# Optimization experiments

Hardware: AMD Instinct MI355X
Metric: run time of the kernel (lower is better)

Reference implementation:

```python
import jax, jax.numpy as jnp
import numpy as np

T, B = 64, 256
VOCAB, D, H = 32000, 512, 1024


def setup_inputs() -> dict:
    key = jax.random.key(0)
    k1, k2, k3, k4 = jax.random.split(key, 4)
    x = jax.random.randint(k1, (T, B), 0, VOCAB)  # token 0 = padding
    embed = jax.random.normal(k2, (VOCAB, D), dtype=jnp.float32)
    w_i = jax.random.normal(k3, (D, 3 * H), dtype=jnp.float32) / np.sqrt(D)
    w_h = jax.random.normal(k4, (H, 3 * H), dtype=jnp.float32) / np.sqrt(H)
    b = jnp.zeros((3 * H,), dtype=jnp.float32)
    return {"x": x, "embed": embed, "w_i": w_i, "w_h": w_h, "b": b}


def reference(x, embed, w_i, w_h, b):
    # Embed and mask out padding token 0.  words: [T, B, D]
    words = embed[x] * (x > 0).astype(embed.dtype)[..., None]
    h_dim = w_h.shape[0]
    w_h_zr, w_h_a = w_h[:, : 2 * h_dim], w_h[:, 2 * h_dim :]
    b_zr, b_a = b[: 2 * h_dim], b[2 * h_dim :]

    def step(h, w_t):
        gx = w_t @ w_i  # [B, 3H]
        zr_x, a_x = gx[..., : 2 * h_dim], gx[..., 2 * h_dim :]
        zr = jax.nn.sigmoid(zr_x + h @ w_h_zr + b_zr)
        z, r = zr[..., :h_dim], zr[..., h_dim:]
        a = jnp.tanh(a_x + (r * h) @ w_h_a + b_a)
        h_new = (1.0 - z) * h + z * a
        return h_new, h_new

    h0 = jnp.zeros((x.shape[1], h_dim), dtype=embed.dtype)
    _, seq = jax.lax.scan(step, h0, words)  # seq: [T, B, H]
    return seq.sum(0)  # compress == 'sum' -> [B, H]
```

## Files before the change

### kernel.cpp

```cpp
#include <hip/hip_runtime.h>
#include <hip/hip_bf16.h>
#include <stdint.h>


#define TT 64
#define BB 256
#define DD 512
#define HH 1024
#define N3H 3072

using frag  = __attribute__((ext_vector_type(8))) short;
using f32x4 = __attribute__((ext_vector_type(4))) float;

__device__ __forceinline__ uint16_t f2b(float f) {
    uint32_t u = __builtin_bit_cast(uint32_t, f);
    uint32_t r = u + 0x7FFFu + ((u >> 16) & 1u);
    return (uint16_t)(r >> 16);
}
__device__ __forceinline__ float b2f(uint16_t b) {
    uint32_t u = ((uint32_t)b) << 16;
    return __builtin_bit_cast(float, u);
}

__device__ __forceinline__ void load8_issue(const uint16_t* p, frag* f) {
    asm volatile(
        "global_load_dwordx4 %0, %8, off sc0 sc1\n\t"
        "global_load_dwordx4 %1, %8, off offset:64 sc0 sc1\n\t"
        "global_load_dwordx4 %2, %8, off offset:128 sc0 sc1\n\t"
        "global_load_dwordx4 %3, %8, off offset:192 sc0 sc1\n\t"
        "global_load_dwordx4 %4, %8, off offset:256 sc0 sc1\n\t"
        "global_load_dwordx4 %5, %8, off offset:320 sc0 sc1\n\t"
        "global_load_dwordx4 %6, %8, off offset:384 sc0 sc1\n\t"
        "global_load_dwordx4 %7, %8, off offset:448 sc0 sc1"
        : "=&v"(f[0]), "=&v"(f[1]), "=&v"(f[2]), "=&v"(f[3]),
          "=&v"(f[4]), "=&v"(f[5]), "=&v"(f[6]), "=&v"(f[7])
        : "v"(p)
        : "memory");
}

#define WAIT8(N, F)                                                       \
    asm volatile("s_waitcnt vmcnt(" #N ")"                                \
                 : "+v"((F)[0]), "+v"((F)[1]), "+v"((F)[2]),              \
                   "+v"((F)[3]), "+v"((F)[4]), "+v"((F)[5]),              \
                   "+v"((F)[6]), "+v"((F)[7]))

#define ZCON(KB, HF)                                                              \
    _Pragma("unroll")                                                             \
    for (int j = 0; j < 8; ++j) {                                                 \
        int kk = (KB) * 8 + j;                                                    \
        frag b0 = *(const frag*)(Wh + (l16)      * LDW + kk * 32 + quad * 8);     \
        frag b1 = *(const frag*)(Wh + (16 + l16) * LDW + kk * 32 + quad * 8);     \
        acc0 = __builtin_amdgcn_mfma_f32_16x16x32_bf16((HF)[j], b0, acc0, 0, 0, 0); \
        acc1 = __builtin_amdgcn_mfma_f32_16x16x32_bf16((HF)[j], b1, acc1, 0, 0, 0); \
    }

#define ACON(KB, RF)                                                              \
    _Pragma("unroll")                                                             \
    for (int j = 0; j < 8; ++j) {                                                 \
        int kk = (KB) * 8 + j;                                                    \
        frag b2 = *(const frag*)(Wh + (32 + l16) * LDW + kk * 32 + quad * 8);     \
        acc2 = __builtin_amdgcn_mfma_f32_16x16x32_bf16((RF)[j], b2, acc2, 0, 0, 0); \
    }


__global__ __launch_bounds__(256) void k_gather(const int* __restrict__ x,
                                                const float* __restrict__ embed,
                                                uint16_t* __restrict__ words) {
    int tid = blockIdx.x * 256 + threadIdx.x;
    int row = tid >> 6;
    int c8  = (tid & 63) << 3;
    int tok = x[row];
    float s = (tok > 0) ? 1.f : 0.f;
    const float4* src = (const float4*)(embed + (int64_t)tok * DD + c8);
    float4 v0 = src[0], v1 = src[1];
    float vals[8] = {v0.x, v0.y, v0.z, v0.w, v1.x, v1.y, v1.z, v1.w};
    union { uint16_t u[8]; uint4 q; } pk;
#pragma unroll
    for (int i = 0; i < 8; ++i) pk.u[i] = f2b(vals[i] * s);
    *(uint4*)(words + ((int64_t)row << 9) + c8) = pk.q;
}

__global__ void k_transpose(const float* __restrict__ src, uint16_t* __restrict__ dst,
                            int K, int N) {
    __shared__ float tile[32][33];
    int n0 = blockIdx.x * 32, k0 = blockIdx.y * 32;
    int tx = threadIdx.x, ty = threadIdx.y;
#pragma unroll
    for (int i = 0; i < 32; i += 8)
        tile[ty + i][tx] = src[(int64_t)(k0 + ty + i) * N + n0 + tx];
    __syncthreads();
#pragma unroll
    for (int i = 0; i < 32; i += 8)
        dst[(int64_t)(n0 + ty + i) * K + k0 + tx] = f2b(tile[tx][ty + i]);
}

__global__ void k_zero(uint4* p, int n16) {
    int i = blockIdx.x * blockDim.x + threadIdx.x;
    if (i < n16) p[i] = uint4{0u, 0u, 0u, 0u};
}


__global__ __launch_bounds__(256) void k_gemm_gx(const uint16_t* __restrict__ A,
                                                 const uint16_t* __restrict__ BT,
                                                 const float* __restrict__ bias,
                                                 uint16_t* __restrict__ C) {
    __shared__ uint16_t As[128][72];
    __shared__ uint16_t Bs[128][72];
    int m0 = blockIdx.y * 128;
    int n0 = blockIdx.x * 128;
    int t = threadIdx.x;
    int wave = t >> 6, lane = t & 63, quad = lane >> 4, l16 = lane & 15;
    int wm = (wave & 1) * 64, wn = (wave >> 1) * 64;
    f32x4 acc[4][4] = {};

    int sr = t >> 1;
    int sc = (t & 1) * 32;

    for (int k0 = 0; k0 < DD; k0 += 64) {
        const uint4* ga = (const uint4*)(A + (int64_t)(m0 + sr) * DD + k0 + sc);
        uint4 a0 = ga[0], a1 = ga[1], a2 = ga[2], a3 = ga[3];
        const uint4* gb = (const uint4*)(BT + (int64_t)(n0 + sr) * DD + k0 + sc);
        uint4 b0 = gb[0], b1 = gb[1], b2 = gb[2], b3 = gb[3];
        __syncthreads();
        *(uint4*)&As[sr][sc]      = a0;
        *(uint4*)&As[sr][sc + 8]  = a1;
        *(uint4*)&As[sr][sc + 16] = a2;
        *(uint4*)&As[sr][sc + 24] = a3;
        *(uint4*)&Bs[sr][sc]      = b0;
        *(uint4*)&Bs[sr][sc + 8]  = b1;
        *(uint4*)&Bs[sr][sc + 16] = b2;
        *(uint4*)&Bs[sr][sc + 24] = b3;
        __syncthreads();
#pragma unroll
        for (int kk = 0; kk < 64; kk += 32) {
            frag af[4], bf[4];
#pragma unroll
            for (int mi = 0; mi < 4; ++mi)
                af[mi] = *(const frag*)&As[wm + mi * 16 + l16][kk + quad * 8];
#pragma unroll
            for (int ni = 0; ni < 4; ++ni)
                bf[ni] = *(const frag*)&Bs[wn + ni * 16 + l16][kk + quad * 8];
#pragma unroll
            for (int mi = 0; mi < 4; ++mi)
#pragma unroll
                for (int ni = 0; ni < 4; ++ni)
                    acc[mi][ni] = __builtin_amdgcn_mfma_f32_16x16x32_bf16(
                        af[mi], bf[ni], acc[mi][ni], 0, 0, 0);
        }
    }
#pragma unroll
    for (int ni = 0; ni < 4; ++ni) {
        int col = n0 + wn + ni * 16 + l16;
        float bv = bias[col];
#pragma unroll
        for (int mi = 0; mi < 4; ++mi)
#pragma unroll
            for (int r = 0; r < 4; ++r) {
                int row = m0 + wm + mi * 16 + quad * 4 + r;
                C[(int64_t)row * N3H + col] = f2b(acc[mi][ni][r] + bv);
            }
    }
}


__global__ __launch_bounds__(256, 1) void k_recur(const uint16_t* __restrict__ gx,
                                                  const uint16_t* __restrict__ wht,
                                                  uint16_t* __restrict__ hbuf,
                                                  uint16_t* __restrict__ rhbuf,
                                                  unsigned int* __restrict__ bar,
                                                  float* __restrict__ out) {
    extern __shared__ uint16_t Wh[];
    const int LDW = HH + 8;
    int mg = blockIdx.x;
    int jb = blockIdx.y;
    int j0 = jb * 16;
    int m0 = mg * 64;
    int t = threadIdx.x, wave = t >> 6, lane = t & 63, quad = lane >> 4, l16 = lane & 15;

    for (int c = t; c < 48 * 128; c += 256) {
        int row = c >> 7;
        int off = (c & 127) << 3;
        int s = row >> 4, i = row & 15;
        *(uint4*)(Wh + row * LDW + off) =
            *(const uint4*)(wht + (int64_t)(s * HH + j0 + i) * HH + off);
    }
    __syncthreads();

    float hp[4]   = {0.f, 0.f, 0.f, 0.f};
    float zg[4];
    float osum[4] = {0.f, 0.f, 0.f, 0.f};
    int brow = m0 + wave * 16 + quad * 4;
    int jcol = j0 + l16;
    const int jc4 = j0 + (l16 & ~3);
    unsigned int* flags = bar + mg * 1024;
    unsigned int phase = 0;

    const uint16_t* harow  = hbuf  + (int64_t)(m0 + wave * 16 + l16) * HH + quad * 8;
    const uint16_t* rharow = rhbuf + (int64_t)(m0 + wave * 16 + l16) * HH + quad * 8;

    auto bar_arrive = [&]() {
        __syncthreads();
        if (t == 0)
            (void)__hip_atomic_fetch_add(&flags[jb * 16], 1u, __ATOMIC_RELAXED,
                                         __HIP_MEMORY_SCOPE_AGENT);
    };
    auto bar_wait = [&](unsigned int ph) {
        if (wave == 0) {
            long guard = 0;
            for (;;) {
                unsigned int v = __hip_atomic_load(&flags[lane * 16], __ATOMIC_RELAXED,
                                                   __HIP_MEMORY_SCOPE_AGENT);
                if (__all((int)(v >= ph))) break;
                __builtin_amdgcn_s_sleep(1);
                if (++guard > (1L << 13)) break;
            }
        }
        __syncthreads();
    };

    auto store4 = [&](uint16_t* base, int r, uint32_t mine) {
        uint32_t p2 = mine | (((uint32_t)__shfl_xor((int)mine, 1)) << 16);
        uint32_t hi = (uint32_t)__shfl_xor((int)p2, 2);
        if ((l16 & 3) == 0) {
            uint64_t p4 = (uint64_t)p2 | ((uint64_t)hi << 32);
            uint64_t* dst = (uint64_t*)base + (int64_t)(brow + r) * (HH / 4) + (jc4 >> 2);
            asm volatile("global_store_dwordx2 %0, %1, off sc0 sc1"
                         :: "v"(dst), "v"(p4) : "memory");
        }
    };

    for (int step = 0; step < TT; ++step) {
        if (step > 0) bar_arrive();

        uint16_t gzv[4], grv[4], gav[4];
        {
            const uint16_t* gxrow = gx + (int64_t)step * BB * N3H;
#pragma unroll
            for (int r = 0; r < 4; ++r) {
                const uint16_t* g = gxrow + (int64_t)(brow + r) * N3H + jcol;
                gzv[r] = g[0]; grv[r] = g[HH]; gav[r] = g[2 * HH];
            }
        }

        if (step > 0) bar_wait(++phase);
        asm volatile("s_waitcnt vmcnt(0)" ::: "memory");

        {
            frag h0[8], h1[8], h2[8], h3[8];
            load8_issue(harow,       h0);
            load8_issue(harow + 256, h1);
            load8_issue(harow + 512, h2);
            load8_issue(harow + 768, h3);
            f32x4 acc0 = {}, acc1 = {};
            WAIT8(24, h0); ZCON(0, h0);
            WAIT8(16, h1); ZCON(1, h1);
            WAIT8(8,  h2); ZCON(2, h2);
            WAIT8(0,  h3); ZCON(3, h3);
#pragma unroll
            for (int r = 0; r < 4; ++r) {
                float zp = b2f(gzv[r]) + acc0[r];
                float rp = b2f(grv[r]) + acc1[r];
                float z  = 1.f / (1.f + __expf(-zp));
                float rg = 1.f / (1.f + __expf(-rp));
                zg[r] = z;
                store4(rhbuf, r, (uint32_t)f2b(rg * hp[r]));
            }
        }

        bar_arrive();
        bar_wait(++phase);
        asm volatile("s_waitcnt vmcnt(0)" ::: "memory");

        {
            frag rf0[8], rf1[8], rf2[8], rf3[8];
            load8_issue(rharow,       rf0);
            load8_issue(rharow + 256, rf1);
            load8_issue(rharow + 512, rf2);
            load8_issue(rharow + 768, rf3);
            f32x4 acc2 = {};
            WAIT8(24, rf0); ACON(0, rf0);
            WAIT8(16, rf1); ACON(1, rf1);
            WAIT8(8,  rf2); ACON(2, rf2);
            WAIT8(0,  rf3); ACON(3, rf3);
#pragma unroll
            for (int r = 0; r < 4; ++r) {
                float a  = tanhf(b2f(gav[r]) + acc2[r]);
                float hn = (1.f - zg[r]) * hp[r] + zg[r] * a;
                osum[r] += hn;
                hp[r] = hn;
                store4(hbuf, r, (uint32_t)f2b(hn));
            }
        }
    }
#pragma unroll
    for (int r = 0; r < 4; ++r)
        out[(int64_t)(brow + r) * HH + jcol] = osum[r];
}


extern "C" void kernel_launch(void* const* d_in, const int* in_sizes, int n_in,
                              void* d_out, int out_size, void* d_ws, size_t ws_size,
                              hipStream_t stream) {
    const int*   x     = (const int*)d_in[0];
    const float* embed = (const float*)d_in[1];
    const float* w_i   = (const float*)d_in[2];
    const float* w_h   = (const float*)d_in[3];
    const float* bias  = (const float*)d_in[4];
    float* out = (float*)d_out;

    char* ws = (char*)d_ws;
    uint16_t* gx    = (uint16_t*)(ws);
    uint16_t* wit   = (uint16_t*)(ws + 100663296);
    uint16_t* wht   = (uint16_t*)(ws + 103809024);
    uint16_t* words = (uint16_t*)(ws + 110100480);
    uint16_t* hbuf  = (uint16_t*)(ws + 126877696);
    uint16_t* rhbuf = (uint16_t*)(ws + 127401984);
    unsigned int* flags = (unsigned int*)(ws + 127926272);

    k_gather<<<4096, 256, 0, stream>>>(x, embed, words);
    k_transpose<<<dim3(96, 16), dim3(32, 8), 0, stream>>>(w_i, wit, DD, N3H);
    k_transpose<<<dim3(96, 32), dim3(32, 8), 0, stream>>>(w_h, wht, HH, N3H);
    k_zero<<<261, 256, 0, stream>>>((uint4*)(ws + 126877696), (1048576 + 16384) / 16);
    k_gemm_gx<<<dim3(24, 128), 256, 0, stream>>>(words, wit, bias, gx);
    k_recur<<<dim3(4, 64), 256, 48 * (HH + 8) * 2, stream>>>(gx, wht, hbuf, rhbuf, flags, out);
}
```

Before: 957.5 us.

## Rotate per-step h and r*h buffers so recurrence loads can use plain cached loads

Adds a templated k_recur path that writes each timestep's h into a fresh slab of a large workspace ring, and r*h into a per-step slab. Because those addresses are never reused, the h and r*h reads become ordinary vector loads instead of sc0/sc1 cache-bypassing inline asm. This also drops the explicit vmcnt(0) waits before them. The aim is to cut the cost of the cross-workgroup exchange between barriers, but it relies on the non-coherent caches never holding stale lines for fresh addresses. The path is used only when the workspace is large enough; otherwise the old path runs.

```diff
diff --git a/kernel.cpp b/kernel.cpp
--- a/kernel.cpp
+++ b/kernel.cpp
@@ -8,6 +8,7 @@
 #define DD 512
 #define HH 1024
 #define N3H 3072
+#define SLAB (BB * HH)
 
 using frag  = __attribute__((ext_vector_type(8))) short;
 using f32x4 = __attribute__((ext_vector_type(4))) float;
@@ -163,10 +164,11 @@
 }
 
 
+template <bool ROT>
 __global__ __launch_bounds__(256, 1) void k_recur(const uint16_t* __restrict__ gx,
                                                   const uint16_t* __restrict__ wht,
-                                                  uint16_t* __restrict__ hbuf,
-                                                  uint16_t* __restrict__ rhbuf,
+                                                  uint16_t* __restrict__ hb,
+                                                  uint16_t* __restrict__ rb,
                                                   unsigned int* __restrict__ bar,
                                                   float* __restrict__ out) {
     extern __shared__ uint16_t Wh[];
@@ -195,8 +197,7 @@
     unsigned int* flags = bar + mg * 1024;
     unsigned int phase = 0;
 
-    const uint16_t* harow  = hbuf  + (int64_t)(m0 + wave * 16 + l16) * HH + quad * 8;
-    const uint16_t* rharow = rhbuf + (int64_t)(m0 + wave * 16 + l16) * HH + quad * 8;
+    const int64_t arow = (int64_t)(m0 + wave * 16 + l16) * HH + quad * 8;
 
     auto bar_arrive = [&]() {
         __syncthreads();
@@ -230,6 +231,17 @@
     };
 
     for (int step = 0; step < TT; ++step) {
+        const uint16_t* hsrc;  uint16_t* rhdst;
+        const uint16_t* rhsrc; uint16_t* hdst;
+        if constexpr (ROT) {
+            hsrc  = hb + (size_t)step * SLAB;
+            hdst  = hb + (size_t)(step + 1) * SLAB;
+            rhsrc = rb + (size_t)step * SLAB;
+            rhdst = rb + (size_t)step * SLAB;
+        } else {
+            hsrc = hb; hdst = hb; rhsrc = rb; rhdst = rb;
+        }
+
         if (step > 0) bar_arrive();
 
         uint16_t gzv[4], grv[4], gav[4];
@@ -243,19 +255,32 @@
         }
 
         if (step > 0) bar_wait(++phase);
-        asm volatile("s_waitcnt vmcnt(0)" ::: "memory");
 
         {
-            frag h0[8], h1[8], h2[8], h3[8];
-            load8_issue(harow,       h0);
-            load8_issue(harow + 256, h1);
-            load8_issue(harow + 512, h2);
-            load8_issue(harow + 768, h3);
             f32x4 acc0 = {}, acc1 = {};
-            WAIT8(24, h0); ZCON(0, h0);
-            WAIT8(16, h1); ZCON(1, h1);
-            WAIT8(8,  h2); ZCON(2, h2);
-            WAIT8(0,  h3); ZCON(3, h3);
+            if constexpr (ROT) {
+                const uint16_t* hrow = hsrc + arow;
+#pragma unroll
+                for (int kb = 0; kb < 4; ++kb) {
+                    frag hf[8];
+#pragma unroll
+                    for (int j = 0; j < 8; ++j)
+                        hf[j] = *(const frag*)(hrow + kb * 256 + j * 32);
+                    ZCON(kb, hf);
+                }
+            } else {
+                asm volatile("s_waitcnt vmcnt(0)" ::: "memory");
+                const uint16_t* hrow = hsrc + arow;
+                frag h0[8], h1[8], h2[8], h3[8];
+                load8_issue(hrow,       h0);
+                load8_issue(hrow + 256, h1);
+                load8_issue(hrow + 512, h2);
+                load8_issue(hrow + 768, h3);
+                WAIT8(24, h0); ZCON(0, h0);
+                WAIT8(16, h1); ZCON(1, h1);
+                WAIT8(8,  h2); ZCON(2, h2);
+                WAIT8(0,  h3); ZCON(3, h3);
+            }
 #pragma unroll
             for (int r = 0; r < 4; ++r) {
                 float zp = b2f(gzv[r]) + acc0[r];
@@ -263,32 +288,45 @@
                 float z  = 1.f / (1.f + __expf(-zp));
                 float rg = 1.f / (1.f + __expf(-rp));
                 zg[r] = z;
-                store4(rhbuf, r, (uint32_t)f2b(rg * hp[r]));
+                store4(rhdst, r, (uint32_t)f2b(rg * hp[r]));
             }
         }
 
         bar_arrive();
         bar_wait(++phase);
-        asm volatile("s_waitcnt vmcnt(0)" ::: "memory");
 
         {
-            frag rf0[8], rf1[8], rf2[8], rf3[8];
-            load8_issue(rharow,       rf0);
-            load8_issue(rharow + 256, rf1);
-            load8_issue(rharow + 512, rf2);
-            load8_issue(rharow + 768, rf3);
             f32x4 acc2 = {};
-            WAIT8(24, rf0); ACON(0, rf0);
-            WAIT8(16, rf1); ACON(1, rf1);
-            WAIT8(8,  rf2); ACON(2, rf2);
-            WAIT8(0,  rf3); ACON(3, rf3);
+            if constexpr (ROT) {
+                const uint16_t* rrow = rhsrc + arow;
+#pragma unroll
+                for (int kb = 0; kb < 4; ++kb) {
+                    frag rf[8];
+#pragma unroll
+                    for (int j = 0; j < 8; ++j)
+                        rf[j] = *(const frag*)(rrow + kb * 256 + j * 32);
+                    ACON(kb, rf);
+                }
+            } else {
+                asm volatile("s_waitcnt vmcnt(0)" ::: "memory");
+                const uint16_t* rrow = rhsrc + arow;
+                frag rf0[8], rf1[8], rf2[8], rf3[8];
+                load8_issue(rrow,       rf0);
+                load8_issue(rrow + 256, rf1);
+                load8_issue(rrow + 512, rf2);
+                load8_issue(rrow + 768, rf3);
+                WAIT8(24, rf0); ACON(0, rf0);
+                WAIT8(16, rf1); ACON(1, rf1);
+                WAIT8(8,  rf2); ACON(2, rf2);
+                WAIT8(0,  rf3); ACON(3, rf3);
+            }
 #pragma unroll
             for (int r = 0; r < 4; ++r) {
                 float a  = tanhf(b2f(gav[r]) + acc2[r]);
                 float hn = (1.f - zg[r]) * hp[r] + zg[r] * a;
                 osum[r] += hn;
                 hp[r] = hn;
-                store4(hbuf, r, (uint32_t)f2b(hn));
+                store4(hdst, r, (uint32_t)f2b(hn));
             }
         }
     }
@@ -316,11 +354,23 @@
     uint16_t* hbuf  = (uint16_t*)(ws + 126877696);
     uint16_t* rhbuf = (uint16_t*)(ws + 127401984);
     unsigned int* flags = (unsigned int*)(ws + 127926272);
+    const size_t ROT_BASE = 127942656;
+    uint16_t* hrot  = (uint16_t*)(ws + ROT_BASE);
+    uint16_t* rhrot = (uint16_t*)(ws + ROT_BASE + 65ull * 524288);
+    const size_t ROT_NEED = ROT_BASE + (65ull + 64ull) * 524288;
+    const bool rot = ws_size >= ROT_NEED;
 
     k_gather<<<4096, 256, 0, stream>>>(x, embed, words);
     k_transpose<<<dim3(96, 16), dim3(32, 8), 0, stream>>>(w_i, wit, DD, N3H);
     k_transpose<<<dim3(96, 32), dim3(32, 8), 0, stream>>>(w_h, wht, HH, N3H);
     k_zero<<<261, 256, 0, stream>>>((uint4*)(ws + 126877696), (1048576 + 16384) / 16);
+    if (rot)
+        k_zero<<<128, 256, 0, stream>>>((uint4*)hrot, 524288 / 16);
     k_gemm_gx<<<dim3(24, 128), 256, 0, stream>>>(words, wit, bias, gx);
-    k_recur<<<dim3(4, 64), 256, 48 * (HH + 8) * 2, stream>>>(gx, wht, hbuf, rhbuf, flags, out);
-}
+    if (rot)
+        k_recur<true><<<dim3(4, 64), 256, 48 * (HH + 8) * 2, stream>>>(
+            gx, wht, hrot, rhrot, flags, out);
+    else
+        k_recur<false><<<dim3(4, 64), 256, 48 * (HH + 8) * 2, stream>>>(
+            gx, wht, hbuf, rhbuf, flags, out);
+}
```

Result: faster. 892.7 us (-6.8%).
